# Optimization experiments

Hardware: AMD Instinct MI355X
Metric: run time of the kernel (lower is better)

The kernel has to match this reference:

```python
import jax, jax.numpy as jnp
import numpy as np
import math

HIDDEN_DIM = 256
NUM_HEADS = 8


def setup_inputs() -> dict:
    key = jax.random.key(0)
    ks = jax.random.split(key, 6)
    B, H, W, C = 2, 64, 64, HIDDEN_DIM
    x = jax.random.normal(ks[0], (B, H, W, C), dtype=jnp.float32)
    w_qkv = jax.random.normal(ks[1], (C, 3 * C), dtype=jnp.float32) * (1.0 / math.sqrt(C))
    b_qkv = jnp.zeros((3 * C,), dtype=jnp.float32)
    w_proj = jax.random.normal(ks[2], (C, C), dtype=jnp.float32) * (1.0 / math.sqrt(C))
    b_proj = jnp.zeros((C,), dtype=jnp.float32)
    # per-head scalar relative bias, shape [num_heads, 1, 1] (init zeros like torch)
    rel_bias = jnp.zeros((NUM_HEADS, 1, 1), dtype=jnp.float32)
    return {"x": x, "w_qkv": w_qkv, "b_qkv": b_qkv, "w_proj": w_proj,
            "b_proj": b_proj, "rel_bias": rel_bias}


def reference(x, w_qkv, b_qkv, w_proj, b_proj, rel_bias):
    B, H, W, C = x.shape
    nh = NUM_HEADS
    hd = C // nh
    N = H * W
    # fused QKV projection: [B, N, 3C]
    qkv = jnp.einsum('bnc,cd->bnd', x.reshape(B, N, C), w_qkv) + b_qkv
    qkv = qkv.reshape(B, N, 3, nh, hd)
    q = jnp.transpose(qkv[:, :, 0], (0, 2, 1, 3))  # [B, nh, N, hd]
    k = jnp.transpose(qkv[:, :, 1], (0, 2, 1, 3))
    v = jnp.transpose(qkv[:, :, 2], (0, 2, 1, 3))
    scale = 1.0 / math.sqrt(hd)
    # full O(N^2) score matrix, per-head scalar bias added pre-softmax
    attn = jnp.einsum('bhnd,bhmd->bhnm', q, k) * scale  # [B, nh, N, N]
    attn = attn + rel_bias[None]  # broadcast [1, nh, 1, 1]
    attn = jax.nn.softmax(attn, axis=-1)
    out = jnp.einsum('bhnm,bhmd->bhnd', attn, v)  # [B, nh, N, hd]
    out = jnp.transpose(out, (0, 2, 1, 3)).reshape(B, H, W, C)
    out = jnp.einsum('bhwc,cd->bhwd', out, w_proj) + b_proj
    return out
```

## Files before the change

kernel.cpp:

```cpp
#include <hip/hip_runtime.h>
#include <math.h>

#define BATCH 2
#define NTOK 4096
#define CDIM 256
#define NH 8
#define HD 32
#define MROWS (BATCH * NTOK)

typedef __attribute__((ext_vector_type(8))) short bf16x8;
typedef __attribute__((ext_vector_type(4))) float f32x4;
typedef __attribute__((ext_vector_type(4))) unsigned u32x4;
typedef unsigned short ushort_t;

union frag_u { uint4 q; u32x4 u; bf16x8 b; };

__device__ __forceinline__ unsigned short f2bf(float f) {
    union { float f; unsigned u; } x; x.f = f;
    unsigned r = x.u + 0x7FFFu + ((x.u >> 16) & 1u);
    return (unsigned short)(r >> 16);
}
__device__ __forceinline__ float bf2f(unsigned short h) {
    union { unsigned u; float f; } x; x.u = ((unsigned)h) << 16; return x.f;
}
__device__ __forceinline__ float exp2_fast(float x) {
    float r;
    asm("v_exp_f32 %0, %1\n\ts_nop 0" : "=v"(r) : "v"(x));
    return r;
}
__device__ __forceinline__ unsigned cvt_pk_bf16(float a, float b) {
    unsigned r;
    asm("v_cvt_pk_bf16_f32 %0, %1, %2" : "=v"(r) : "v"(a), "v"(b));
    return r;
}
__device__ __forceinline__ float max3f(float a, float b, float c) {
    float r;
    asm("v_max3_f32 %0, %1, %2, %3" : "=v"(r) : "v"(a), "v"(b), "v"(c));
    return r;
}
__device__ __forceinline__ unsigned pk_f16_rne(float a, float b) {
    union { _Float16 h[2]; unsigned u; } r;
    r.h[0] = (_Float16)a; r.h[1] = (_Float16)b;
    return r.u;
}
__device__ __forceinline__ void permlane_pv(unsigned &a, unsigned &b) {
    asm("s_nop 1\n\t"
        "v_permlane32_swap_b32 %0, %1\n\t"
        "s_nop 1\n\t"
        "v_permlane16_swap_b32 %0, %1" : "+v"(a), "+v"(b));
}

__global__ __launch_bounds__(256) void prep_wt(
    const float* __restrict__ W, ushort_t* __restrict__ Whi, ushort_t* __restrict__ Wlo,
    int K, int N)
{
    __shared__ float T[32][33];
    const int tid = threadIdx.x;
    const int n0 = blockIdx.x * 32, k0 = blockIdx.y * 32;
    const int r = tid >> 3, c4 = (tid & 7) << 2;
    float4 v = *(const float4*)&W[(size_t)(k0 + r) * N + n0 + c4];
    T[r][c4 + 0] = v.x; T[r][c4 + 1] = v.y; T[r][c4 + 2] = v.z; T[r][c4 + 3] = v.w;
    __syncthreads();
    float f0 = T[c4 + 0][r], f1 = T[c4 + 1][r], f2 = T[c4 + 2][r], f3 = T[c4 + 3][r];
    unsigned h01 = cvt_pk_bf16(f0, f1), h23 = cvt_pk_bf16(f2, f3);
    union { unsigned u; float f; } a, b;
    a.u = h01 << 16; b.u = h01 & 0xFFFF0000u;
    unsigned l01 = cvt_pk_bf16(f0 - a.f, f1 - b.f);
    a.u = h23 << 16; b.u = h23 & 0xFFFF0000u;
    unsigned l23 = cvt_pk_bf16(f2 - a.f, f3 - b.f);
    size_t o = (size_t)(n0 + r) * K + k0 + c4;
    *(uint2*)&Whi[o] = make_uint2(h01, h23);
    *(uint2*)&Wlo[o] = make_uint2(l01, l23);
}

__global__ __launch_bounds__(256) void qkv_mfma(
    const float* __restrict__ X,
    const ushort_t* __restrict__ Wthi, const ushort_t* __restrict__ Wtlo,
    const float* __restrict__ bias,
    ushort_t* __restrict__ Qhi, ushort_t* __restrict__ Qlo,
    ushort_t* __restrict__ Khi, ushort_t* __restrict__ Vhi)
{
    __shared__ __align__(16) ushort_t Ah[64][40], Al[64][40], Bh[64][40], Bl[64][40];

    const int tid = threadIdx.x;
    const int w = tid >> 6, lane = tid & 63, lq = lane & 15, g = lane >> 4;
    const int wm = w >> 1, wn = w & 1;
    const int row0 = blockIdx.x * 64, col0 = blockIdx.y * 64;
    const int sr = tid >> 2, sc = (tid & 3) << 3;

    f32x4 acc[2][2] = {};

    for (int k0 = 0; k0 < CDIM; k0 += 32) {
        __syncthreads();
        {
            float4 xa = *(const float4*)&X[(size_t)(row0 + sr) * CDIM + k0 + sc];
            float4 xb = *(const float4*)&X[(size_t)(row0 + sr) * CDIM + k0 + sc + 4];
            unsigned h01 = cvt_pk_bf16(xa.x, xa.y), h23 = cvt_pk_bf16(xa.z, xa.w);
            unsigned h45 = cvt_pk_bf16(xb.x, xb.y), h67 = cvt_pk_bf16(xb.z, xb.w);
            union { unsigned u; float f; } t0, t1;
            t0.u = h01 << 16; t1.u = h01 & 0xFFFF0000u;
            unsigned l01 = cvt_pk_bf16(xa.x - t0.f, xa.y - t1.f);
            t0.u = h23 << 16; t1.u = h23 & 0xFFFF0000u;
            unsigned l23 = cvt_pk_bf16(xa.z - t0.f, xa.w - t1.f);
            t0.u = h45 << 16; t1.u = h45 & 0xFFFF0000u;
            unsigned l45 = cvt_pk_bf16(xb.x - t0.f, xb.y - t1.f);
            t0.u = h67 << 16; t1.u = h67 & 0xFFFF0000u;
            unsigned l67 = cvt_pk_bf16(xb.z - t0.f, xb.w - t1.f);
            *(uint4*)&Ah[sr][sc] = make_uint4(h01, h23, h45, h67);
            *(uint4*)&Al[sr][sc] = make_uint4(l01, l23, l45, l67);
            *(uint4*)&Bh[sr][sc] = *(const uint4*)&Wthi[(size_t)(col0 + sr) * CDIM + k0 + sc];
            *(uint4*)&Bl[sr][sc] = *(const uint4*)&Wtlo[(size_t)(col0 + sr) * CDIM + k0 + sc];
        }
        __syncthreads();

        bf16x8 ah[2], al[2], bh[2], bl[2];
        #pragma unroll
        for (int i = 0; i < 2; ++i) {
            ah[i] = *(const bf16x8*)&Ah[wm * 32 + i * 16 + lq][g * 8];
            al[i] = *(const bf16x8*)&Al[wm * 32 + i * 16 + lq][g * 8];
        }
        #pragma unroll
        for (int j = 0; j < 2; ++j) {
            bh[j] = *(const bf16x8*)&Bh[wn * 32 + j * 16 + lq][g * 8];
            bl[j] = *(const bf16x8*)&Bl[wn * 32 + j * 16 + lq][g * 8];
        }
        #pragma unroll
        for (int i = 0; i < 2; ++i)
            #pragma unroll
            for (int j = 0; j < 2; ++j) {
                acc[i][j] = __builtin_amdgcn_mfma_f32_16x16x32_bf16(ah[i], bh[j], acc[i][j], 0, 0, 0);
                acc[i][j] = __builtin_amdgcn_mfma_f32_16x16x32_bf16(ah[i], bl[j], acc[i][j], 0, 0, 0);
                acc[i][j] = __builtin_amdgcn_mfma_f32_16x16x32_bf16(al[i], bh[j], acc[i][j], 0, 0, 0);
            }
    }

    const int s = col0 >> 8;
    const int b_ = row0 >> 12;
    const int nb0 = (row0 & (NTOK - 1)) + wm * 32 + 4 * g;
    const float QSC = (float)(1.4426950408889634 / 5.656854249492381);

    #pragma unroll
    for (int j = 0; j < 2; ++j) {
        const int gcol = col0 + wn * 32 + j * 16 + lq;
        const float bv = bias[gcol];
        const int h = (gcol >> 5) & 7, e = gcol & 31;
        const int bh_ = b_ * NH + h;
        #pragma unroll
        for (int i = 0; i < 2; ++i) {
            #pragma unroll
            for (int r = 0; r < 4; ++r) {
                const int n = nb0 + i * 16 + r;
                float val = acc[i][j][r] + bv;
                if (s == 0) {
                    val *= QSC;
                    unsigned short hh = f2bf(val);
                    unsigned short ll = f2bf(val - bf2f(hh));
                    size_t idx = ((size_t)bh_ * NTOK + n) * HD + e;
                    Qhi[idx] = hh; Qlo[idx] = ll;
                } else if (s == 1) {
                    Khi[((size_t)bh_ * NTOK + n) * HD + e] = f2bf(val);
                } else {
                    Vhi[((size_t)bh_ * HD + e) * NTOK + n] = f2bf(val);
                }
            }
        }
    }
}

__global__ __launch_bounds__(256, 3) void attn_v17(
    const ushort_t* __restrict__ Qhi, const ushort_t* __restrict__ Qlo,
    const ushort_t* __restrict__ Khi, const ushort_t* __restrict__ Vhi,
    ushort_t* __restrict__ P_O, float* __restrict__ P_l, float* __restrict__ P_m)
{
    __shared__ __align__(16) ushort_t KH[64][44];
    __shared__ __align__(16) ushort_t VH[32][68];

    const int tid = threadIdx.x;
    const int w = tid >> 6, lane = tid & 63, lq = lane & 15, g = lane >> 4;
    const int bx = blockIdx.x;
    const int bh = bx & 15, qc = (bx >> 4) & 63, hf = bx >> 10;
    const int q0 = qc * 64 + w * 16;
    const int kb = bh * (NTOK * HD);
    const int vb = bh * (HD * NTOK);

    bf16x8 qh, ql;
    {
        const int qi = kb + (q0 + lq) * HD + g * 8;
        qh = *(const bf16x8*)(Qhi + qi);
        ql = *(const bf16x8*)(Qlo + qi);
    }

    const bf16x8 vones = {0x3F80, 0x3F80, 0x3F80, 0x3F80, 0x3F80, 0x3F80, 0x3F80, 0x3F80};

    const int kr = tid >> 2, kc = (tid & 3) << 3;
    const int vr = tid >> 3, vc = (tid & 7) << 3;
    const ushort_t* pKH = Khi + kb + (hf * 2048 + kr) * HD + kc;
    const ushort_t* pVH = Vhi + vb + vr * NTOK + hf * 2048 + vc;

    uint4 sKH = *(const uint4*)pKH;  pKH += 64 * HD;
    uint4 sVH = *(const uint4*)pVH;  pVH += 64;

    f32x4 o0 = {}, o1 = {};
    f32x4 lfrag = {};
    float m_ = -1e30f;

    for (int step = 0; step < 32; ++step) {
        __syncthreads();
        *(uint4*)&KH[kr][kc] = sKH;
        *(uint4*)&VH[vr][vc] = sVH;
        __syncthreads();

        sKH = *(const uint4*)pKH;  pKH += 64 * HD;
        sVH = *(const uint4*)pVH;  pVH += 64;

        bf16x8 kh[4];
        #pragma unroll
        for (int t = 0; t < 4; ++t)
            kh[t] = *(const bf16x8*)&KH[16 * t + lq][g * 8];

        f32x4 sc[4];
        __builtin_amdgcn_s_setprio(1);
        #pragma unroll
        for (int t = 0; t < 4; ++t) {
            f32x4 cc = {0.f, 0.f, 0.f, 0.f};
            cc = __builtin_amdgcn_mfma_f32_16x16x32_bf16(kh[t], qh, cc, 0, 0, 0);
            cc = __builtin_amdgcn_mfma_f32_16x16x32_bf16(kh[t], ql, cc, 0, 0, 0);
            sc[t] = cc;
        }
        __builtin_amdgcn_s_setprio(0);

        float a0 = max3f(sc[0][0], sc[0][1], sc[0][2]);
        float a1 = max3f(sc[0][3], sc[1][0], sc[1][1]);
        float a2 = max3f(sc[1][2], sc[1][3], sc[2][0]);
        float a3 = max3f(sc[2][1], sc[2][2], sc[2][3]);
        float a4 = max3f(sc[3][0], sc[3][1], sc[3][2]);
        float b0 = max3f(a0, a1, a2);
        float b1 = max3f(a3, a4, sc[3][3]);
        float mx = fmaxf(b0, b1);
        mx = fmaxf(mx, __shfl_xor(mx, 16));
        mx = fmaxf(mx, __shfl_xor(mx, 32));

        if (!__all(mx <= m_ + 8.0f)) {
            float mnew = fmaxf(m_, mx);
            float rs = exp2_fast(m_ - mnew);
            m_ = mnew;
            lfrag *= rs;
            o0 *= rs;
            o1 *= rs;
        }

        unsigned ph[4][2];
        #pragma unroll
        for (int t = 0; t < 4; ++t) {
            float p0 = exp2_fast(sc[t][0] - m_);
            float p1 = exp2_fast(sc[t][1] - m_);
            float p2 = exp2_fast(sc[t][2] - m_);
            float p3 = exp2_fast(sc[t][3] - m_);
            ph[t][0] = cvt_pk_bf16(p0, p1);
            ph[t][1] = cvt_pk_bf16(p2, p3);
        }

        #pragma unroll
        for (int ks = 0; ks < 2; ++ks) {
            unsigned h00 = ph[2 * ks][0], h10 = ph[2 * ks + 1][0];
            unsigned h01 = ph[2 * ks][1], h11 = ph[2 * ks + 1][1];
            permlane_pv(h00, h10);
            permlane_pv(h01, h11);
            frag_u PH; PH.u = (u32x4){h00, h01, h10, h11};
            bf16x8 v0f = *(const bf16x8*)&VH[lq][ks * 32 + g * 8];
            bf16x8 v1f = *(const bf16x8*)&VH[16 + lq][ks * 32 + g * 8];
            __builtin_amdgcn_s_setprio(1);
            o0 = __builtin_amdgcn_mfma_f32_16x16x32_bf16(v0f, PH.b, o0, 0, 0, 0);
            o1 = __builtin_amdgcn_mfma_f32_16x16x32_bf16(v1f, PH.b, o1, 0, 0, 0);
            lfrag = __builtin_amdgcn_mfma_f32_16x16x32_bf16(vones, PH.b, lfrag, 0, 0, 0);
            __builtin_amdgcn_s_setprio(0);
        }
    }

    const float ls = lfrag[0];

    const float invl = 1.0f / ls;
    const int qg = q0 + lq;
    const size_t prow = ((size_t)(hf * 16 + bh) * NTOK + qg);
    {
        unsigned w0 = pk_f16_rne(o0[0] * invl, o0[1] * invl);
        unsigned w1 = pk_f16_rne(o0[2] * invl, o0[3] * invl);
        *(uint2*)&P_O[prow * 32 + 4 * g] = make_uint2(w0, w1);
        unsigned w2 = pk_f16_rne(o1[0] * invl, o1[1] * invl);
        unsigned w3 = pk_f16_rne(o1[2] * invl, o1[3] * invl);
        *(uint2*)&P_O[prow * 32 + 16 + 4 * g] = make_uint2(w2, w3);
    }
    if (g == 0) {
        P_l[prow] = ls;
        P_m[prow] = m_;
    }
}

__global__ __launch_bounds__(256) void merge_norm(
    const ushort_t* __restrict__ P_O, const float* __restrict__ P_l,
    const float* __restrict__ P_m,
    ushort_t* __restrict__ AOhi, ushort_t* __restrict__ AOlo)
{
    const int t = blockIdx.x * 256 + threadIdx.x;
    const int bhq = t >> 2;
    const int dq = (t & 3) << 3;
    union { uint4 q; _Float16 h[8]; } a, b;
    a.q = *(const uint4*)&P_O[(size_t)bhq * 32 + dq];
    b.q = *(const uint4*)&P_O[(size_t)(65536 + bhq) * 32 + dq];
    const float l0 = P_l[bhq], l1 = P_l[65536 + bhq];
    const float m0 = P_m[bhq], m1 = P_m[65536 + bhq];
    const float mstar = fmaxf(m0, m1);
    const float w0r = exp2_fast(m0 - mstar) * l0;
    const float w1r = exp2_fast(m1 - mstar) * l1;
    const float inv = 1.0f / (w0r + w1r);
    const float w0 = w0r * inv, w1 = w1r * inv;
    const int bh = bhq >> 12, q = bhq & 4095;
    const size_t ob = ((size_t)(bh >> 3) * NTOK + q) * CDIM + (bh & 7) * 32 + dq;

    float f[8];
    #pragma unroll
    for (int i = 0; i < 8; ++i) f[i] = (float)a.h[i] * w0 + (float)b.h[i] * w1;

    unsigned h01 = cvt_pk_bf16(f[0], f[1]), h23 = cvt_pk_bf16(f[2], f[3]);
    unsigned h45 = cvt_pk_bf16(f[4], f[5]), h67 = cvt_pk_bf16(f[6], f[7]);
    union { unsigned u; float ff; } x, y;
    x.u = h01 << 16; y.u = h01 & 0xFFFF0000u;
    unsigned l01 = cvt_pk_bf16(f[0] - x.ff, f[1] - y.ff);
    x.u = h23 << 16; y.u = h23 & 0xFFFF0000u;
    unsigned l23 = cvt_pk_bf16(f[2] - x.ff, f[3] - y.ff);
    x.u = h45 << 16; y.u = h45 & 0xFFFF0000u;
    unsigned l45 = cvt_pk_bf16(f[4] - x.ff, f[5] - y.ff);
    x.u = h67 << 16; y.u = h67 & 0xFFFF0000u;
    unsigned l67 = cvt_pk_bf16(f[6] - x.ff, f[7] - y.ff);

    *(uint4*)&AOhi[ob] = make_uint4(h01, h23, h45, h67);
    *(uint4*)&AOlo[ob] = make_uint4(l01, l23, l45, l67);
}

__global__ __launch_bounds__(256) void proj_mfma(
    const ushort_t* __restrict__ AOhi, const ushort_t* __restrict__ AOlo,
    const ushort_t* __restrict__ Wthi, const ushort_t* __restrict__ Wtlo,
    const float* __restrict__ bias, float* __restrict__ out)
{
    __shared__ __align__(16) ushort_t Ah[64][40], Al[64][40], Bh[64][40], Bl[64][40];

    const int tid = threadIdx.x;
    const int w = tid >> 6, lane = tid & 63, lq = lane & 15, g = lane >> 4;
    const int wm = w >> 1, wn = w & 1;
    const int row0 = blockIdx.x * 64, col0 = blockIdx.y * 64;
    const int sr = tid >> 2, sc = (tid & 3) << 3;

    f32x4 acc[2][2] = {};

    for (int k0 = 0; k0 < CDIM; k0 += 32) {
        __syncthreads();
        *(uint4*)&Ah[sr][sc] = *(const uint4*)&AOhi[(size_t)(row0 + sr) * CDIM + k0 + sc];
        *(uint4*)&Al[sr][sc] = *(const uint4*)&AOlo[(size_t)(row0 + sr) * CDIM + k0 + sc];
        *(uint4*)&Bh[sr][sc] = *(const uint4*)&Wthi[(size_t)(col0 + sr) * CDIM + k0 + sc];
        *(uint4*)&Bl[sr][sc] = *(const uint4*)&Wtlo[(size_t)(col0 + sr) * CDIM + k0 + sc];
        __syncthreads();

        bf16x8 ah[2], al[2], bh[2], bl[2];
        #pragma unroll
        for (int i = 0; i < 2; ++i) {
            ah[i] = *(const bf16x8*)&Ah[wm * 32 + i * 16 + lq][g * 8];
            al[i] = *(const bf16x8*)&Al[wm * 32 + i * 16 + lq][g * 8];
        }
        #pragma unroll
        for (int j = 0; j < 2; ++j) {
            bh[j] = *(const bf16x8*)&Bh[wn * 32 + j * 16 + lq][g * 8];
            bl[j] = *(const bf16x8*)&Bl[wn * 32 + j * 16 + lq][g * 8];
        }
        #pragma unroll
        for (int i = 0; i < 2; ++i)
            #pragma unroll
            for (int j = 0; j < 2; ++j) {
                acc[i][j] = __builtin_amdgcn_mfma_f32_16x16x32_bf16(ah[i], bh[j], acc[i][j], 0, 0, 0);
                acc[i][j] = __builtin_amdgcn_mfma_f32_16x16x32_bf16(ah[i], bl[j], acc[i][j], 0, 0, 0);
                acc[i][j] = __builtin_amdgcn_mfma_f32_16x16x32_bf16(al[i], bh[j], acc[i][j], 0, 0, 0);
            }
    }

    #pragma unroll
    for (int j = 0; j < 2; ++j) {
        const int gcol = col0 + wn * 32 + j * 16 + lq;
        const float bv = bias[gcol];
        #pragma unroll
        for (int i = 0; i < 2; ++i) {
            #pragma unroll
            for (int r = 0; r < 4; ++r) {
                const int grow = row0 + wm * 32 + i * 16 + 4 * g + r;
                out[(size_t)grow * CDIM + gcol] = acc[i][j][r] + bv;
            }
        }
    }
}

extern "C" void kernel_launch(void* const* d_in, const int* in_sizes, int n_in,
                              void* d_out, int out_size, void* d_ws, size_t ws_size,
                              hipStream_t stream)
{
    const float* x      = (const float*)d_in[0];
    const float* w_qkv  = (const float*)d_in[1];
    const float* b_qkv  = (const float*)d_in[2];
    const float* w_proj = (const float*)d_in[3];
    const float* b_proj = (const float*)d_in[4];

    float* out = (float*)d_out;

    char* p = (char*)d_ws;
    ushort_t* Qhi   = (ushort_t*)(p);
    ushort_t* Qlo   = (ushort_t*)(p + 4194304);
    ushort_t* Khi   = (ushort_t*)(p + 8388608);
    ushort_t* Vhi   = (ushort_t*)(p + 12582912);
    ushort_t* Wqthi = (ushort_t*)(p + 16777216);
    ushort_t* Wqtlo = (ushort_t*)(p + 16777216 + 393216);
    ushort_t* Wpthi = (ushort_t*)(p + 16777216 + 786432);
    ushort_t* Wptlo = (ushort_t*)(p + 16777216 + 917504);
    ushort_t* P_O   = (ushort_t*)(p + 17825792);
    float*    P_l   = (float*)(p + 26214400);
    float*    P_m   = (float*)(p + 26738688);
    ushort_t* AOhi  = Khi;
    ushort_t* AOlo  = Vhi;

    prep_wt<<<dim3(24, 8), 256, 0, stream>>>(w_qkv, Wqthi, Wqtlo, 256, 768);
    prep_wt<<<dim3(8, 8), 256, 0, stream>>>(w_proj, Wpthi, Wptlo, 256, 256);

    qkv_mfma<<<dim3(MROWS / 64, 768 / 64), 256, 0, stream>>>(
        x, Wqthi, Wqtlo, b_qkv, Qhi, Qlo, Khi, Vhi);

    attn_v17<<<2048, 256, 0, stream>>>(Qhi, Qlo, Khi, Vhi, P_O, P_l, P_m);

    merge_norm<<<1024, 256, 0, stream>>>(P_O, P_l, P_m, AOhi, AOlo);

    proj_mfma<<<dim3(MROWS / 64, CDIM / 64), 256, 0, stream>>>(
        AOhi, AOlo, Wpthi, Wptlo, b_proj, out);
}
```

Measured before the change: 127.5 us.

## Drop Q low-part split and stage 128-key tiles per barrier pair

Q is now stored as a single bf16 value instead of a hi/lo pair, which halves the QK^T MFMAs in the attention kernel and removes the Qlo write and read. The attention loop also stages 128 keys per shared-memory fill and processes them in two 64-key passes, halving the number of __syncthreads and global load rounds. In exchange, score precision drops to plain bf16 Q, and the larger LDS tiles may reduce occupancy.

After: 121.3 us. 1.05x faster.

```diff
diff --git a/kernel.cpp b/kernel.cpp
--- a/kernel.cpp
+++ b/kernel.cpp
@@ -77,8 +77,7 @@
     const float* __restrict__ X,
     const ushort_t* __restrict__ Wthi, const ushort_t* __restrict__ Wtlo,
     const float* __restrict__ bias,
-    ushort_t* __restrict__ Qhi, ushort_t* __restrict__ Qlo,
-    ushort_t* __restrict__ Khi, ushort_t* __restrict__ Vhi)
+    ushort_t* __restrict__ Qhi, ushort_t* __restrict__ Khi, ushort_t* __restrict__ Vhi)
 {
     __shared__ __align__(16) ushort_t Ah[64][40], Al[64][40], Bh[64][40], Bl[64][40];
 
@@ -152,11 +151,7 @@
                 const int n = nb0 + i * 16 + r;
                 float val = acc[i][j][r] + bv;
                 if (s == 0) {
-                    val *= QSC;
-                    unsigned short hh = f2bf(val);
-                    unsigned short ll = f2bf(val - bf2f(hh));
-                    size_t idx = ((size_t)bh_ * NTOK + n) * HD + e;
-                    Qhi[idx] = hh; Qlo[idx] = ll;
+                    Qhi[((size_t)bh_ * NTOK + n) * HD + e] = f2bf(val * QSC);
                 } else if (s == 1) {
                     Khi[((size_t)bh_ * NTOK + n) * HD + e] = f2bf(val);
                 } else {
@@ -167,13 +162,13 @@
     }
 }
 
-__global__ __launch_bounds__(256, 3) void attn_v17(
-    const ushort_t* __restrict__ Qhi, const ushort_t* __restrict__ Qlo,
+__global__ __launch_bounds__(256, 3) void attn_v19(
+    const ushort_t* __restrict__ Qhi,
     const ushort_t* __restrict__ Khi, const ushort_t* __restrict__ Vhi,
     ushort_t* __restrict__ P_O, float* __restrict__ P_l, float* __restrict__ P_m)
 {
-    __shared__ __align__(16) ushort_t KH[64][44];
-    __shared__ __align__(16) ushort_t VH[32][68];
+    __shared__ __align__(16) ushort_t KH[128][44];
+    __shared__ __align__(16) ushort_t VH[32][132];
 
     const int tid = threadIdx.x;
     const int w = tid >> 6, lane = tid & 63, lq = lane & 15, g = lane >> 4;
@@ -183,97 +178,107 @@
     const int kb = bh * (NTOK * HD);
     const int vb = bh * (HD * NTOK);
 
-    bf16x8 qh, ql;
+    bf16x8 qh;
     {
         const int qi = kb + (q0 + lq) * HD + g * 8;
         qh = *(const bf16x8*)(Qhi + qi);
-        ql = *(const bf16x8*)(Qlo + qi);
     }
 
     const bf16x8 vones = {0x3F80, 0x3F80, 0x3F80, 0x3F80, 0x3F80, 0x3F80, 0x3F80, 0x3F80};
 
-    const int kr = tid >> 2, kc = (tid & 3) << 3;
-    const int vr = tid >> 3, vc = (tid & 7) << 3;
-    const ushort_t* pKH = Khi + kb + (hf * 2048 + kr) * HD + kc;
-    const ushort_t* pVH = Vhi + vb + vr * NTOK + hf * 2048 + vc;
-
-    uint4 sKH = *(const uint4*)pKH;  pKH += 64 * HD;
-    uint4 sVH = *(const uint4*)pVH;  pVH += 64;
+    const int kr0 = tid >> 2,          kc0 = (tid & 3) << 3;
+    const int kr1 = (tid + 256) >> 2,  kc1 = ((tid + 256) & 3) << 3;
+    const int vr0 = tid >> 4,          vc0 = (tid & 15) << 3;
+    const int vr1 = (tid + 256) >> 4,  vc1 = ((tid + 256) & 15) << 3;
+    const ushort_t* pK0 = Khi + kb + (hf * 2048 + kr0) * HD + kc0;
+    const ushort_t* pK1 = Khi + kb + (hf * 2048 + kr1) * HD + kc1;
+    const ushort_t* pV0 = Vhi + vb + vr0 * NTOK + hf * 2048 + vc0;
+    const ushort_t* pV1 = Vhi + vb + vr1 * NTOK + hf * 2048 + vc1;
+
+    uint4 sK0 = *(const uint4*)pK0;  pK0 += 128 * HD;
+    uint4 sK1 = *(const uint4*)pK1;  pK1 += 128 * HD;
+    uint4 sV0 = *(const uint4*)pV0;  pV0 += 128;
+    uint4 sV1 = *(const uint4*)pV1;  pV1 += 128;
 
     f32x4 o0 = {}, o1 = {};
     f32x4 lfrag = {};
     float m_ = -1e30f;
 
-    for (int step = 0; step < 32; ++step) {
-        __syncthreads();
-        *(uint4*)&KH[kr][kc] = sKH;
-        *(uint4*)&VH[vr][vc] = sVH;
-        __syncthreads();
-
-        sKH = *(const uint4*)pKH;  pKH += 64 * HD;
-        sVH = *(const uint4*)pVH;  pVH += 64;
-
-        bf16x8 kh[4];
-        #pragma unroll
-        for (int t = 0; t < 4; ++t)
-            kh[t] = *(const bf16x8*)&KH[16 * t + lq][g * 8];
-
-        f32x4 sc[4];
-        __builtin_amdgcn_s_setprio(1);
-        #pragma unroll
-        for (int t = 0; t < 4; ++t) {
-            f32x4 cc = {0.f, 0.f, 0.f, 0.f};
-            cc = __builtin_amdgcn_mfma_f32_16x16x32_bf16(kh[t], qh, cc, 0, 0, 0);
-            cc = __builtin_amdgcn_mfma_f32_16x16x32_bf16(kh[t], ql, cc, 0, 0, 0);
-            sc[t] = cc;
-        }
-        __builtin_amdgcn_s_setprio(0);
-
-        float a0 = max3f(sc[0][0], sc[0][1], sc[0][2]);
-        float a1 = max3f(sc[0][3], sc[1][0], sc[1][1]);
-        float a2 = max3f(sc[1][2], sc[1][3], sc[2][0]);
-        float a3 = max3f(sc[2][1], sc[2][2], sc[2][3]);
-        float a4 = max3f(sc[3][0], sc[3][1], sc[3][2]);
-        float b0 = max3f(a0, a1, a2);
-        float b1 = max3f(a3, a4, sc[3][3]);
-        float mx = fmaxf(b0, b1);
-        mx = fmaxf(mx, __shfl_xor(mx, 16));
-        mx = fmaxf(mx, __shfl_xor(mx, 32));
-
-        if (!__all(mx <= m_ + 8.0f)) {
-            float mnew = fmaxf(m_, mx);
-            float rs = exp2_fast(m_ - mnew);
-            m_ = mnew;
-            lfrag *= rs;
-            o0 *= rs;
-            o1 *= rs;
-        }
-
-        unsigned ph[4][2];
-        #pragma unroll
-        for (int t = 0; t < 4; ++t) {
-            float p0 = exp2_fast(sc[t][0] - m_);
-            float p1 = exp2_fast(sc[t][1] - m_);
-            float p2 = exp2_fast(sc[t][2] - m_);
-            float p3 = exp2_fast(sc[t][3] - m_);
-            ph[t][0] = cvt_pk_bf16(p0, p1);
-            ph[t][1] = cvt_pk_bf16(p2, p3);
-        }
-
-        #pragma unroll
-        for (int ks = 0; ks < 2; ++ks) {
-            unsigned h00 = ph[2 * ks][0], h10 = ph[2 * ks + 1][0];
-            unsigned h01 = ph[2 * ks][1], h11 = ph[2 * ks + 1][1];
-            permlane_pv(h00, h10);
-            permlane_pv(h01, h11);
-            frag_u PH; PH.u = (u32x4){h00, h01, h10, h11};
-            bf16x8 v0f = *(const bf16x8*)&VH[lq][ks * 32 + g * 8];
-            bf16x8 v1f = *(const bf16x8*)&VH[16 + lq][ks * 32 + g * 8];
+    for (int stage = 0; stage < 16; ++stage) {
+        __syncthreads();
+        *(uint4*)&KH[kr0][kc0] = sK0;
+        *(uint4*)&KH[kr1][kc1] = sK1;
+        *(uint4*)&VH[vr0][vc0] = sV0;
+        *(uint4*)&VH[vr1][vc1] = sV1;
+        __syncthreads();
+
+        sK0 = *(const uint4*)pK0;  pK0 += 128 * HD;
+        sK1 = *(const uint4*)pK1;  pK1 += 128 * HD;
+        sV0 = *(const uint4*)pV0;  pV0 += 128;
+        sV1 = *(const uint4*)pV1;  pV1 += 128;
+
+        #pragma unroll
+        for (int pass = 0; pass < 2; ++pass) {
+            bf16x8 kh[4];
+            #pragma unroll
+            for (int t = 0; t < 4; ++t)
+                kh[t] = *(const bf16x8*)&KH[pass * 64 + 16 * t + lq][g * 8];
+
+            f32x4 sc[4];
             __builtin_amdgcn_s_setprio(1);
-            o0 = __builtin_amdgcn_mfma_f32_16x16x32_bf16(v0f, PH.b, o0, 0, 0, 0);
-            o1 = __builtin_amdgcn_mfma_f32_16x16x32_bf16(v1f, PH.b, o1, 0, 0, 0);
-            lfrag = __builtin_amdgcn_mfma_f32_16x16x32_bf16(vones, PH.b, lfrag, 0, 0, 0);
+            #pragma unroll
+            for (int t = 0; t < 4; ++t) {
+                f32x4 cc = {0.f, 0.f, 0.f, 0.f};
+                sc[t] = __builtin_amdgcn_mfma_f32_16x16x32_bf16(kh[t], qh, cc, 0, 0, 0);
+            }
             __builtin_amdgcn_s_setprio(0);
+
+            float a0 = max3f(sc[0][0], sc[0][1], sc[0][2]);
+            float a1 = max3f(sc[0][3], sc[1][0], sc[1][1]);
+            float a2 = max3f(sc[1][2], sc[1][3], sc[2][0]);
+            float a3 = max3f(sc[2][1], sc[2][2], sc[2][3]);
+            float a4 = max3f(sc[3][0], sc[3][1], sc[3][2]);
+            float b0 = max3f(a0, a1, a2);
+            float b1 = max3f(a3, a4, sc[3][3]);
+            float mx = fmaxf(b0, b1);
+            mx = fmaxf(mx, __shfl_xor(mx, 16));
+            mx = fmaxf(mx, __shfl_xor(mx, 32));
+
+            if (!__all(mx <= m_ + 8.0f)) {
+                float mnew = fmaxf(m_, mx);
+                float rs = exp2_fast(m_ - mnew);
+                m_ = mnew;
+                lfrag *= rs;
+                o0 *= rs;
+                o1 *= rs;
+            }
+
+            unsigned ph[4][2];
+            #pragma unroll
+            for (int t = 0; t < 4; ++t) {
+                float p0 = exp2_fast(sc[t][0] - m_);
+                float p1 = exp2_fast(sc[t][1] - m_);
+                float p2 = exp2_fast(sc[t][2] - m_);
+                float p3 = exp2_fast(sc[t][3] - m_);
+                ph[t][0] = cvt_pk_bf16(p0, p1);
+                ph[t][1] = cvt_pk_bf16(p2, p3);
+            }
+
+            #pragma unroll
+            for (int ks = 0; ks < 2; ++ks) {
+                unsigned h00 = ph[2 * ks][0], h10 = ph[2 * ks + 1][0];
+                unsigned h01 = ph[2 * ks][1], h11 = ph[2 * ks + 1][1];
+                permlane_pv(h00, h10);
+                permlane_pv(h01, h11);
+                frag_u PH; PH.u = (u32x4){h00, h01, h10, h11};
+                bf16x8 v0f = *(const bf16x8*)&VH[lq][pass * 64 + ks * 32 + g * 8];
+                bf16x8 v1f = *(const bf16x8*)&VH[16 + lq][pass * 64 + ks * 32 + g * 8];
+                __builtin_amdgcn_s_setprio(1);
+                o0 = __builtin_amdgcn_mfma_f32_16x16x32_bf16(v0f, PH.b, o0, 0, 0, 0);
+                o1 = __builtin_amdgcn_mfma_f32_16x16x32_bf16(v1f, PH.b, o1, 0, 0, 0);
+                lfrag = __builtin_amdgcn_mfma_f32_16x16x32_bf16(vones, PH.b, lfrag, 0, 0, 0);
+                __builtin_amdgcn_s_setprio(0);
+            }
         }
     }
 
@@ -410,16 +415,15 @@
 
     char* p = (char*)d_ws;
     ushort_t* Qhi   = (ushort_t*)(p);
-    ushort_t* Qlo   = (ushort_t*)(p + 4194304);
-    ushort_t* Khi   = (ushort_t*)(p + 8388608);
-    ushort_t* Vhi   = (ushort_t*)(p + 12582912);
-    ushort_t* Wqthi = (ushort_t*)(p + 16777216);
-    ushort_t* Wqtlo = (ushort_t*)(p + 16777216 + 393216);
-    ushort_t* Wpthi = (ushort_t*)(p + 16777216 + 786432);
-    ushort_t* Wptlo = (ushort_t*)(p + 16777216 + 917504);
-    ushort_t* P_O   = (ushort_t*)(p + 17825792);
-    float*    P_l   = (float*)(p + 26214400);
-    float*    P_m   = (float*)(p + 26738688);
+    ushort_t* Khi   = (ushort_t*)(p + 4194304);
+    ushort_t* Vhi   = (ushort_t*)(p + 8388608);
+    ushort_t* Wqthi = (ushort_t*)(p + 12582912);
+    ushort_t* Wqtlo = (ushort_t*)(p + 12582912 + 393216);
+    ushort_t* Wpthi = (ushort_t*)(p + 12582912 + 786432);
+    ushort_t* Wptlo = (ushort_t*)(p + 12582912 + 917504);
+    ushort_t* P_O   = (ushort_t*)(p + 13631488);
+    float*    P_l   = (float*)(p + 22020096);
+    float*    P_m   = (float*)(p + 22544384);
     ushort_t* AOhi  = Khi;
     ushort_t* AOlo  = Vhi;
 
@@ -427,9 +431,9 @@
     prep_wt<<<dim3(8, 8), 256, 0, stream>>>(w_proj, Wpthi, Wptlo, 256, 256);
 
     qkv_mfma<<<dim3(MROWS / 64, 768 / 64), 256, 0, stream>>>(
-        x, Wqthi, Wqtlo, b_qkv, Qhi, Qlo, Khi, Vhi);
-
-    attn_v17<<<2048, 256, 0, stream>>>(Qhi, Qlo, Khi, Vhi, P_O, P_l, P_m);
+        x, Wqthi, Wqtlo, b_qkv, Qhi, Khi, Vhi);
+
+    attn_v19<<<2048, 256, 0, stream>>>(Qhi, Khi, Vhi, P_O, P_l, P_m);
 
     merge_norm<<<1024, 256, 0, stream>>>(P_O, P_l, P_m, AOhi, AOlo);
 
```
